# Performance work log

Measured on AMD Instinct MI355X. Metric: run time of the kernel, lower is better.

The kernel has to match this reference:

```python
import jax, jax.numpy as jnp
import numpy as np

DIV_VAL = 11.313708498984761  # sqrt(128), the softmax temperature used as div_val


def setup_inputs() -> dict:
    key = jax.random.key(0)
    kq, kk, kv = jax.random.split(key, 3)
    B, Lq, Lk, D = 16, 4096, 4096, 128
    return {
        "query": jax.random.normal(kq, (B, Lq, D), dtype=jnp.float32),
        "key": jax.random.normal(kk, (B, Lk, D), dtype=jnp.float32),
        "value": jax.random.normal(kv, (B, Lk, D), dtype=jnp.float32),
    }


def reference(query, key, value):
    # qk = Q @ K^T, scaled by 1/div_val  -> [B, Lq, Lk]
    scaled_qk = jnp.einsum("bqd,bkd->bqk", query, key) / DIV_VAL
    # numerically stable softmax over last axis; dropout is identity (eval / p=0)
    attn = jax.nn.softmax(scaled_qk, axis=-1)
    # output = attn @ V -> [B, Lq, Dv]
    return jnp.einsum("bqk,bkd->bqd", attn, value)
```

## Files before the change

### kernel.cpp

```cpp
#include <hip/hip_runtime.h>

#define B_  16
#define L_  4096
#define D_  128
#define NT2 (L_ / 128)

typedef __attribute__((ext_vector_type(8)))  __bf16 bf16x8;
typedef __attribute__((ext_vector_type(2)))  __bf16 bf16x2;
typedef __attribute__((ext_vector_type(16))) float  f32x16;
typedef __attribute__((ext_vector_type(4)))  float  f32x4;
typedef __attribute__((ext_vector_type(4)))  int    i32x4;
typedef __attribute__((ext_vector_type(8)))  unsigned short u16x8;
typedef __attribute__((ext_vector_type(4)))  unsigned short u16x4;

#ifndef __has_builtin
#define __has_builtin(x) 0
#endif
#if __has_builtin(__builtin_amdgcn_permlane32_swap)
#define HAVE_PLSWAP 1
#else
#define HAVE_PLSWAP 0
#endif

__device__ __forceinline__ unsigned short f2bf(float f){
  unsigned u = __builtin_bit_cast(unsigned, f);
  u += 0x7fffu + ((u >> 16) & 1u);
  return (unsigned short)(u >> 16);
}

__device__ __forceinline__ int packbf(float a, float b){
  bf16x2 t; t[0] = (__bf16)a; t[1] = (__bf16)b;
  return __builtin_bit_cast(int, t);
}

__device__ __forceinline__ void gload16(const void* g, void* l){
  __builtin_amdgcn_global_load_lds(
      (const __attribute__((address_space(1))) unsigned int*)g,
      (__attribute__((address_space(3))) unsigned int*)l, 16, 0, 0);
}

__device__ __forceinline__ f32x16 z16(){
  f32x16 t;
#pragma unroll
  for (int i = 0; i < 16; ++i) t[i] = 0.f;
  return t;
}

__global__ void cvt_bf16_kernel(const float* __restrict__ in,
                                unsigned short* __restrict__ out, int n8,
                                float scale){
  int i = blockIdx.x * blockDim.x + threadIdx.x;
  if (i >= n8) return;
  const float4* p = reinterpret_cast<const float4*>(in) + (size_t)i * 2;
  float4 a = p[0], b = p[1];
  u16x8 o;
  o[0]=f2bf(a.x*scale); o[1]=f2bf(a.y*scale); o[2]=f2bf(a.z*scale); o[3]=f2bf(a.w*scale);
  o[4]=f2bf(b.x*scale); o[5]=f2bf(b.y*scale); o[6]=f2bf(b.z*scale); o[7]=f2bf(b.w*scale);
  reinterpret_cast<u16x8*>(out)[i] = o;
}

__global__ void transpose_v_kernel(const float* __restrict__ V,
                                   unsigned short* __restrict__ Vt){
  __shared__ unsigned short tile[64][65];
  const int k0 = blockIdx.x * 64, d0 = blockIdx.y * 64, b = blockIdx.z;
  const int tr = threadIdx.x >> 4, tc = threadIdx.x & 15;
  const float* src = V + ((size_t)b * L_ + k0) * D_ + d0;
#pragma unroll
  for (int p = 0; p < 4; ++p){
    int kl = p * 16 + tr;
    float4 v = *reinterpret_cast<const float4*>(src + (size_t)kl * D_ + tc * 4);
    tile[kl][tc*4+0] = f2bf(v.x);
    tile[kl][tc*4+1] = f2bf(v.y);
    tile[kl][tc*4+2] = f2bf(v.z);
    tile[kl][tc*4+3] = f2bf(v.w);
  }
  __syncthreads();
  unsigned short* dst = Vt + (size_t)b * D_ * L_ + (size_t)d0 * L_ + k0;
#pragma unroll
  for (int p = 0; p < 4; ++p){
    int dl = p * 16 + tr;
    u16x4 o;
    o[0] = tile[tc*4+0][dl];
    o[1] = tile[tc*4+1][dl];
    o[2] = tile[tc*4+2][dl];
    o[3] = tile[tc*4+3][dl];
    *reinterpret_cast<u16x4*>(dst + (size_t)dl * L_ + tc * 4) = o;
  }
}

__device__ __forceinline__ bf16x8 mkchunk(float a0,float a1,float a2,float a3,
                                          float a4,float a5,float a6,float a7,
                                          int hi){
  int x0 = packbf(a0,a1), x1 = packbf(a2,a3);
  int x2 = packbf(a4,a5), x3 = packbf(a6,a7);
  int W0, W1, W2, W3;
#if HAVE_PLSWAP
  {
    auto r = __builtin_amdgcn_permlane32_swap((unsigned)x0, (unsigned)x2, false, false);
    W0 = (int)r[0]; W2 = (int)r[1];
  }
  {
    auto r = __builtin_amdgcn_permlane32_swap((unsigned)x1, (unsigned)x3, false, false);
    W1 = (int)r[0]; W3 = (int)r[1];
  }
  (void)hi;
#else
  int y0 = __shfl_xor(x0, 32), y1 = __shfl_xor(x1, 32);
  int y2 = __shfl_xor(x2, 32), y3 = __shfl_xor(x3, 32);
  W0 = hi ? y2 : x0;  W1 = hi ? y3 : x1;
  W2 = hi ? x2 : y0;  W3 = hi ? x3 : y1;
#endif
  i32x4 ww; ww[0]=W0; ww[1]=W1; ww[2]=W2; ww[3]=W3;
  return __builtin_bit_cast(bf16x8, ww);
}

__global__ __launch_bounds__(512, 1)
void attn_kernel(const float* __restrict__ Q,
                 const unsigned short* __restrict__ Kb,
                 const unsigned short* __restrict__ Vt,
                 float* __restrict__ out){
  __shared__ char smem[131072];
  char* Klds = smem;
  char* Vlds = smem + 65536;

  const int tid = threadIdx.x;
  const int w = tid >> 6, l = tid & 63;
  const int row = l & 31, hi = l >> 5;
  const int swz = (row & 15) << 4;
  const int b = blockIdx.x, qt = blockIdx.y;

  const float* qptr = Q + ((size_t)b * L_ + (size_t)qt * 256 + w * 32 + row) * D_;
  bf16x8 qf[8];
#pragma unroll
  for (int c = 0; c < 8; ++c){
    float4 a  = *reinterpret_cast<const float4*>(qptr + c * 16 + hi * 8);
    float4 bb = *reinterpret_cast<const float4*>(qptr + c * 16 + hi * 8 + 4);
    u16x8 o;
    o[0]=f2bf(a.x);  o[1]=f2bf(a.y);  o[2]=f2bf(a.z);  o[3]=f2bf(a.w);
    o[4]=f2bf(bb.x); o[5]=f2bf(bb.y); o[6]=f2bf(bb.z); o[7]=f2bf(bb.w);
    qf[c] = __builtin_bit_cast(bf16x8, o);
  }

  const char* Kg = (const char*)(Kb + (size_t)b * L_ * D_);
  const char* Vg = (const char*)(Vt + (size_t)b * (size_t)D_ * L_);

  f32x16 o[4];
#pragma unroll
  for (int n = 0; n < 4; ++n) o[n] = z16();
  float ln = 0.f;

  auto STAGE = [&](int bsel, int t){
    char* kd = Klds + bsel * 32768;
    char* vd = Vlds + bsel * 32768;
    const int kv0 = t * 128;
#pragma unroll
    for (int j = 0; j < 4; ++j){
      int idx = j * 512 + tid;
      int kr = idx >> 4, sc = idx & 15;
      int clog = (sc << 4) ^ ((kr & 15) << 4);
      gload16(Kg + (size_t)(kv0 + kr) * 256 + clog, kd + idx * 16);
    }
#pragma unroll
    for (int j = 0; j < 4; ++j){
      int idx = j * 512 + tid;
      int dr = idx >> 4, sc = idx & 15;
      int clog = (sc << 4) ^ ((dr & 15) << 4);
      gload16(Vg + (size_t)dr * (L_ * 2) + (size_t)kv0 * 2 + clog, vd + idx * 16);
    }
  };

#define QKTH(C0, C1, KC, H)                                                    \
  {                                                                            \
    const char* Kc_ = (KC);                                                    \
    C0 = z16(); C1 = z16();                                                    \
    __builtin_amdgcn_s_setprio(1);                                             \
    _Pragma("unroll")                                                          \
    for (int c = 0; c < 8; ++c){                                               \
      bf16x8 kf0 = *(const bf16x8*)(Kc_ + ((H)*64 + row) * 256 +               \
                                    ((c*32 + hi*16) ^ swz));                   \
      bf16x8 kf1 = *(const bf16x8*)(Kc_ + ((H)*64 + row + 32) * 256 +          \
                                    ((c*32 + hi*16) ^ swz));                   \
      C0 = __builtin_amdgcn_mfma_f32_32x32x16_bf16(kf0, qf[c], C0, 0, 0, 0);   \
      C1 = __builtin_amdgcn_mfma_f32_32x32x16_bf16(kf1, qf[c], C1, 0, 0, 0);   \
    }                                                                          \
    __builtin_amdgcn_s_setprio(0);                                             \
  }

#define SMPACK(P0, P1)                                                         \
    _Pragma("unroll")                                                          \
    for (int i2 = 0; i2 < 16; ++i2){                                           \
      P0[i2] = __builtin_amdgcn_exp2f(P0[i2]);                                 \
      P1[i2] = __builtin_amdgcn_exp2f(P1[i2]);                                 \
    }                                                                          \
    {                                                                          \
      f32x16 pt_ = P0 + P1;                                                    \
      float a0 = pt_[0]+pt_[1],  a1 = pt_[2]+pt_[3];                           \
      float a2 = pt_[4]+pt_[5],  a3 = pt_[6]+pt_[7];                           \
      float a4 = pt_[8]+pt_[9],  a5 = pt_[10]+pt_[11];                         \
      float a6 = pt_[12]+pt_[13], a7 = pt_[14]+pt_[15];                        \
      ln += ((a0+a1)+(a2+a3)) + ((a4+a5)+(a6+a7));                             \
    }                                                                          \
    bf16x8 pa0 = mkchunk(P0[0],P0[1],P0[2],P0[3],P0[4],P0[5],P0[6],P0[7], hi); \
    bf16x8 pa1 = mkchunk(P0[8],P0[9],P0[10],P0[11],P0[12],P0[13],P0[14],P0[15], hi); \
    bf16x8 pa2 = mkchunk(P1[0],P1[1],P1[2],P1[3],P1[4],P1[5],P1[6],P1[7], hi); \
    bf16x8 pa3 = mkchunk(P1[8],P1[9],P1[10],P1[11],P1[12],P1[13],P1[14],P1[15], hi);

#define PVH(VP, H)                                                             \
  {                                                                            \
    const char* Vp_ = (VP);                                                    \
    __builtin_amdgcn_s_setprio(1);                                             \
    _Pragma("unroll")                                                          \
    for (int n2 = 0; n2 < 4; ++n2){                                            \
      const char* vr_ = Vp_ + (n2 * 32 + row) * 256;                           \
      bf16x8 vf0 = *(const bf16x8*)(vr_ + ((((H)*4+0)*32 + hi*16) ^ swz));     \
      bf16x8 vf1 = *(const bf16x8*)(vr_ + ((((H)*4+1)*32 + hi*16) ^ swz));     \
      bf16x8 vf2 = *(const bf16x8*)(vr_ + ((((H)*4+2)*32 + hi*16) ^ swz));     \
      bf16x8 vf3 = *(const bf16x8*)(vr_ + ((((H)*4+3)*32 + hi*16) ^ swz));     \
      o[n2] = __builtin_amdgcn_mfma_f32_32x32x16_bf16(vf0, pa0, o[n2], 0,0,0); \
      o[n2] = __builtin_amdgcn_mfma_f32_32x32x16_bf16(vf1, pa1, o[n2], 0,0,0); \
      o[n2] = __builtin_amdgcn_mfma_f32_32x32x16_bf16(vf2, pa2, o[n2], 0,0,0); \
      o[n2] = __builtin_amdgcn_mfma_f32_32x32x16_bf16(vf3, pa3, o[n2], 0,0,0); \
    }                                                                          \
    __builtin_amdgcn_s_setprio(0);                                             \
  }

  STAGE(0, 0);
  asm volatile("s_waitcnt vmcnt(0)" ::: "memory");
  __builtin_amdgcn_s_barrier();
  int cur = 0;

  f32x16 sA0, sA1, sB0, sB1;
  for (int i = 0; i < NT2; ++i){
    if (i + 1 < NT2) STAGE(cur ^ 1, i + 1);

    const char* Kc = Klds + cur * 32768;
    const char* Vc = Vlds + cur * 32768;

    QKTH(sA0, sA1, Kc, 0);
    QKTH(sB0, sB1, Kc, 1);
    { SMPACK(sA0, sA1) PVH(Vc, 0) }
    { SMPACK(sB0, sB1) PVH(Vc, 1) }

    asm volatile("s_waitcnt vmcnt(0)" ::: "memory");
    __builtin_amdgcn_s_barrier();
    cur ^= 1;
  }

  float lt = ln + __shfl_xor(ln, 32);
  float inv = 1.0f / lt;
  float* outp = out + ((size_t)b * L_ + (size_t)qt * 256 + w * 32 + row) * D_;
#pragma unroll
  for (int n = 0; n < 4; ++n)
#pragma unroll
    for (int rq = 0; rq < 4; ++rq){
      f32x4 v4;
      v4[0] = o[n][rq*4+0] * inv;
      v4[1] = o[n][rq*4+1] * inv;
      v4[2] = o[n][rq*4+2] * inv;
      v4[3] = o[n][rq*4+3] * inv;
      *reinterpret_cast<f32x4*>(outp + n * 32 + rq * 8 + hi * 4) = v4;
    }
}

extern "C" void kernel_launch(void* const* d_in, const int* in_sizes, int n_in,
                              void* d_out, int out_size, void* d_ws, size_t ws_size,
                              hipStream_t stream){
  const float* Q = (const float*)d_in[0];
  const float* K = (const float*)d_in[1];
  const float* V = (const float*)d_in[2];
  float* out = (float*)d_out;

  const size_t NE = (size_t)B_ * L_ * D_;
  unsigned short* kb = (unsigned short*)d_ws;
  unsigned short* vt = kb + NE;

  const float SCALE_L2E = 1.4426950408889634f / 11.313708498984761f;
  int n8 = (int)(NE / 8);
  cvt_bf16_kernel<<<dim3(n8 / 256), 256, 0, stream>>>(K, kb, n8, SCALE_L2E);
  transpose_v_kernel<<<dim3(L_ / 64, D_ / 64, B_), 256, 0, stream>>>(V, vt);
  attn_kernel<<<dim3(B_, L_ / 256), 512, 0, stream>>>(Q, kb, vt, out);
}
```

Before: 172.6 us.

## Split block into two ping-pong wave groups over alternating KV tiles

The block now handles 128 query rows instead of 256 and splits its 8 waves into two groups of 4, each processing alternate 64-key tiles. While one group runs QK^T MFMAs, the other runs softmax and PV, which overlaps exp/pack work with matrix work. A 4-slot LDS ring holds the tiles. The two partial outputs and row sums are combined through LDS at the end. Grid size doubles, and each K/V tile is reused by fewer queries, so global traffic per query increases.

```diff
diff --git a/kernel.cpp b/kernel.cpp
--- a/kernel.cpp
+++ b/kernel.cpp
@@ -3,7 +3,7 @@
 #define B_  16
 #define L_  4096
 #define D_  128
-#define NT2 (L_ / 128)
+#define NS  32
 
 typedef __attribute__((ext_vector_type(8)))  __bf16 bf16x8;
 typedef __attribute__((ext_vector_type(2)))  __bf16 bf16x2;
@@ -125,11 +125,13 @@
 
   const int tid = threadIdx.x;
   const int w = tid >> 6, l = tid & 63;
+  const int grp = w >> 2, wq = w & 3;
+  const int gtid = tid & 255;
   const int row = l & 31, hi = l >> 5;
   const int swz = (row & 15) << 4;
   const int b = blockIdx.x, qt = blockIdx.y;
 
-  const float* qptr = Q + ((size_t)b * L_ + (size_t)qt * 256 + w * 32 + row) * D_;
+  const float* qptr = Q + ((size_t)b * L_ + (size_t)qt * 128 + wq * 32 + row) * D_;
   bf16x8 qf[8];
 #pragma unroll
   for (int c = 0; c < 8; ++c){
@@ -150,36 +152,36 @@
   float ln = 0.f;
 
   auto STAGE = [&](int bsel, int t){
-    char* kd = Klds + bsel * 32768;
-    char* vd = Vlds + bsel * 32768;
-    const int kv0 = t * 128;
+    char* kd = Klds + bsel * 16384;
+    char* vd = Vlds + bsel * 16384;
+    const int kv0 = t * 64;
 #pragma unroll
     for (int j = 0; j < 4; ++j){
-      int idx = j * 512 + tid;
+      int idx = j * 256 + gtid;
       int kr = idx >> 4, sc = idx & 15;
       int clog = (sc << 4) ^ ((kr & 15) << 4);
       gload16(Kg + (size_t)(kv0 + kr) * 256 + clog, kd + idx * 16);
     }
 #pragma unroll
     for (int j = 0; j < 4; ++j){
-      int idx = j * 512 + tid;
-      int dr = idx >> 4, sc = idx & 15;
-      int clog = (sc << 4) ^ ((dr & 15) << 4);
-      gload16(Vg + (size_t)dr * (L_ * 2) + (size_t)kv0 * 2 + clog, vd + idx * 16);
+      int idx = j * 256 + gtid;
+      int lr = idx >> 4, sc = idx & 15;
+      int clog = (sc << 4) ^ ((lr & 15) << 4);
+      int dd = lr + ((clog >> 7) << 6);
+      gload16(Vg + (size_t)dd * (L_ * 2) + (size_t)kv0 * 2 + (clog & 127),
+              vd + idx * 16);
     }
   };
 
-#define QKTH(C0, C1, KC, H)                                                    \
+#define QKT(C0, C1, KC)                                                        \
   {                                                                            \
     const char* Kc_ = (KC);                                                    \
     C0 = z16(); C1 = z16();                                                    \
     __builtin_amdgcn_s_setprio(1);                                             \
     _Pragma("unroll")                                                          \
     for (int c = 0; c < 8; ++c){                                               \
-      bf16x8 kf0 = *(const bf16x8*)(Kc_ + ((H)*64 + row) * 256 +               \
-                                    ((c*32 + hi*16) ^ swz));                   \
-      bf16x8 kf1 = *(const bf16x8*)(Kc_ + ((H)*64 + row + 32) * 256 +          \
-                                    ((c*32 + hi*16) ^ swz));                   \
+      bf16x8 kf0 = *(const bf16x8*)(Kc_ + row * 256 + ((c*32 + hi*16) ^ swz)); \
+      bf16x8 kf1 = *(const bf16x8*)(Kc_ + (row+32) * 256 + ((c*32 + hi*16) ^ swz)); \
       C0 = __builtin_amdgcn_mfma_f32_32x32x16_bf16(kf0, qf[c], C0, 0, 0, 0);   \
       C1 = __builtin_amdgcn_mfma_f32_32x32x16_bf16(kf1, qf[c], C1, 0, 0, 0);   \
     }                                                                          \
@@ -205,17 +207,20 @@
     bf16x8 pa2 = mkchunk(P1[0],P1[1],P1[2],P1[3],P1[4],P1[5],P1[6],P1[7], hi); \
     bf16x8 pa3 = mkchunk(P1[8],P1[9],P1[10],P1[11],P1[12],P1[13],P1[14],P1[15], hi);
 
-#define PVH(VP, H)                                                             \
+#define VF(VP, N, CH)                                                          \
+  (*(const bf16x8*)((VP) + ((N & 1) * 32 + row) * 256 +                        \
+                    ((((N >> 1) * 128) + (CH)*32 + hi*16) ^ swz)))
+
+#define PVH(VP)                                                                \
   {                                                                            \
     const char* Vp_ = (VP);                                                    \
     __builtin_amdgcn_s_setprio(1);                                             \
     _Pragma("unroll")                                                          \
     for (int n2 = 0; n2 < 4; ++n2){                                            \
-      const char* vr_ = Vp_ + (n2 * 32 + row) * 256;                           \
-      bf16x8 vf0 = *(const bf16x8*)(vr_ + ((((H)*4+0)*32 + hi*16) ^ swz));     \
-      bf16x8 vf1 = *(const bf16x8*)(vr_ + ((((H)*4+1)*32 + hi*16) ^ swz));     \
-      bf16x8 vf2 = *(const bf16x8*)(vr_ + ((((H)*4+2)*32 + hi*16) ^ swz));     \
-      bf16x8 vf3 = *(const bf16x8*)(vr_ + ((((H)*4+3)*32 + hi*16) ^ swz));     \
+      bf16x8 vf0 = VF(Vp_, n2, 0);                                             \
+      bf16x8 vf1 = VF(Vp_, n2, 1);                                             \
+      bf16x8 vf2 = VF(Vp_, n2, 2);                                             \
+      bf16x8 vf3 = VF(Vp_, n2, 3);                                             \
       o[n2] = __builtin_amdgcn_mfma_f32_32x32x16_bf16(vf0, pa0, o[n2], 0,0,0); \
       o[n2] = __builtin_amdgcn_mfma_f32_32x32x16_bf16(vf1, pa1, o[n2], 0,0,0); \
       o[n2] = __builtin_amdgcn_mfma_f32_32x32x16_bf16(vf2, pa2, o[n2], 0,0,0); \
@@ -224,42 +229,66 @@
     __builtin_amdgcn_s_setprio(0);                                             \
   }
 
-  STAGE(0, 0);
+  if (grp == 0) STAGE(0, 0); else STAGE(1, 1);
   asm volatile("s_waitcnt vmcnt(0)" ::: "memory");
   __builtin_amdgcn_s_barrier();
-  int cur = 0;
-
-  f32x16 sA0, sA1, sB0, sB1;
-  for (int i = 0; i < NT2; ++i){
-    if (i + 1 < NT2) STAGE(cur ^ 1, i + 1);
-
-    const char* Kc = Klds + cur * 32768;
-    const char* Vc = Vlds + cur * 32768;
-
-    QKTH(sA0, sA1, Kc, 0);
-    QKTH(sB0, sB1, Kc, 1);
-    { SMPACK(sA0, sA1) PVH(Vc, 0) }
-    { SMPACK(sB0, sB1) PVH(Vc, 1) }
-
-    asm volatile("s_waitcnt vmcnt(0)" ::: "memory");
+
+  f32x16 S0, S1;
+  for (int s = 0; s < NS; ++s){
+    if (grp == 0){
+      if (s < NS - 1) STAGE((2*s + 2) & 3, 2*s + 2);
+      QKT(S0, S1, Klds + ((2*s) & 3) * 16384);
+    } else {
+      if (s > 0){ SMPACK(S0, S1) PVH(Vlds + ((2*s - 1) & 3) * 16384) }
+      asm volatile("s_waitcnt vmcnt(0)" ::: "memory");
+    }
     __builtin_amdgcn_s_barrier();
-    cur ^= 1;
-  }
-
-  float lt = ln + __shfl_xor(ln, 32);
-  float inv = 1.0f / lt;
-  float* outp = out + ((size_t)b * L_ + (size_t)qt * 256 + w * 32 + row) * D_;
-#pragma unroll
-  for (int n = 0; n < 4; ++n)
-#pragma unroll
-    for (int rq = 0; rq < 4; ++rq){
-      f32x4 v4;
-      v4[0] = o[n][rq*4+0] * inv;
-      v4[1] = o[n][rq*4+1] * inv;
-      v4[2] = o[n][rq*4+2] * inv;
-      v4[3] = o[n][rq*4+3] * inv;
-      *reinterpret_cast<f32x4*>(outp + n * 32 + rq * 8 + hi * 4) = v4;
+
+    if (grp == 0){
+      { SMPACK(S0, S1) PVH(Vlds + ((2*s) & 3) * 16384) }
+      asm volatile("s_waitcnt vmcnt(0)" ::: "memory");
+    } else {
+      if (s < NS - 1) STAGE((2*s + 3) & 3, 2*s + 3);
+      QKT(S0, S1, Klds + ((2*s + 1) & 3) * 16384);
     }
+    __builtin_amdgcn_s_barrier();
+  }
+  if (grp == 1){ SMPACK(S0, S1) PVH(Vlds + 3 * 16384) }
+  __builtin_amdgcn_s_barrier();
+
+  float4* xbuf = (float4*)smem;
+  float*  lnbuf = (float*)(smem + 65536);
+  const int slot = wq * 64 + l;
+  if (grp == 1){
+#pragma unroll
+    for (int n = 0; n < 4; ++n)
+#pragma unroll
+      for (int rq = 0; rq < 4; ++rq){
+        f32x4 v4;
+        v4[0]=o[n][rq*4+0]; v4[1]=o[n][rq*4+1]; v4[2]=o[n][rq*4+2]; v4[3]=o[n][rq*4+3];
+        xbuf[slot * 16 + n * 4 + rq] = *(float4*)&v4;
+      }
+    lnbuf[slot] = ln;
+  }
+  __builtin_amdgcn_s_barrier();
+  if (grp == 0){
+    ln += lnbuf[slot];
+    float lt = ln + __shfl_xor(ln, 32);
+    float inv = 1.0f / lt;
+    float* outp = out + ((size_t)b * L_ + (size_t)qt * 128 + wq * 32 + row) * D_;
+#pragma unroll
+    for (int n = 0; n < 4; ++n)
+#pragma unroll
+      for (int rq = 0; rq < 4; ++rq){
+        float4 q4 = xbuf[slot * 16 + n * 4 + rq];
+        f32x4 v4;
+        v4[0] = (o[n][rq*4+0] + q4.x) * inv;
+        v4[1] = (o[n][rq*4+1] + q4.y) * inv;
+        v4[2] = (o[n][rq*4+2] + q4.z) * inv;
+        v4[3] = (o[n][rq*4+3] + q4.w) * inv;
+        *reinterpret_cast<f32x4*>(outp + n * 32 + rq * 8 + hi * 4) = v4;
+      }
+  }
 }
 
 extern "C" void kernel_launch(void* const* d_in, const int* in_sizes, int n_in,
@@ -278,5 +307,5 @@
   int n8 = (int)(NE / 8);
   cvt_bf16_kernel<<<dim3(n8 / 256), 256, 0, stream>>>(K, kb, n8, SCALE_L2E);
   transpose_v_kernel<<<dim3(L_ / 64, D_ / 64, B_), 256, 0, stream>>>(V, vt);
-  attn_kernel<<<dim3(B_, L_ / 256), 512, 0, stream>>>(Q, kb, vt, out);
-}
+  attn_kernel<<<dim3(B_, L_ / 128), 512, 0, stream>>>(Q, kb, vt, out);
+}
```

Result: slower. 201.7 us (+16.9%).
